# Kernel tuning notes

Hardware: AMD Instinct MI355X
Metric: run time of the kernel (lower is better)

The kernel has to match this reference:

```python
import jax, jax.numpy as jnp
import numpy as np

N = 100000
E = 1600000
D_IN = 128
HEADS = 4
C = 16  # hidden // heads
NEG_SLOPE = 0.2


def setup_inputs() -> dict:
    key = jax.random.key(0)
    ks = jax.random.split(key, 8)
    x = jax.random.normal(ks[0], (N, D_IN), dtype=jnp.float32)
    edge_index = jax.random.randint(ks[1], (2, E), 0, N, dtype=jnp.int32)
    s = 1.0 / np.sqrt(D_IN)
    W_l = jax.random.normal(ks[2], (D_IN, HEADS * C), dtype=jnp.float32) * s
    b_l = jnp.zeros((HEADS * C,), dtype=jnp.float32)
    W_r = jax.random.normal(ks[3], (D_IN, HEADS * C), dtype=jnp.float32) * s
    b_r = jnp.zeros((HEADS * C,), dtype=jnp.float32)
    att = jax.random.normal(ks[4], (HEADS, C), dtype=jnp.float32) * (1.0 / np.sqrt(C))
    bias = jnp.zeros((HEADS * C,), dtype=jnp.float32)
    W_head = jax.random.normal(ks[5], (HEADS * C, 1), dtype=jnp.float32) * (1.0 / np.sqrt(HEADS * C))
    b_head = jnp.zeros((1,), dtype=jnp.float32)
    return {"x": x, "edge_index": edge_index, "W_l": W_l, "b_l": b_l,
            "W_r": W_r, "b_r": b_r, "att": att, "bias": bias,
            "W_head": W_head, "b_head": b_head}


def reference(x, edge_index, W_l, b_l, W_r, b_r, att, bias, W_head, b_head):
    # GATv2Conv (PyG semantics, add_self_loops=True, concat=True)
    n = x.shape[0]
    # add self loops
    loops = jnp.arange(n, dtype=edge_index.dtype)
    src = jnp.concatenate([edge_index[0], loops])  # source j
    dst = jnp.concatenate([edge_index[1], loops])  # target i
    # per-node linear projections -> [N, H, C]
    x_l = (x @ W_l + b_l).reshape(n, HEADS, C)
    x_r = (x @ W_r + b_r).reshape(n, HEADS, C)
    # per-edge attention logits: att . LeakyReLU(x_l[j] + x_r[i])
    e = x_l[src] + x_r[dst]                               # [E', H, C]
    e = jnp.where(e >= 0, e, NEG_SLOPE * e)
    logits = jnp.einsum('ehc,hc->eh', e, att)             # [E', H]
    # segment softmax over incoming edges of each target node
    seg_max = jax.ops.segment_max(logits, dst, num_segments=n)  # [N, H]
    expw = jnp.exp(logits - seg_max[dst])
    seg_sum = jax.ops.segment_sum(expw, dst, num_segments=n)
    alpha = expw / seg_sum[dst]                           # [E', H]
    # weighted scatter-aggregate of source messages
    msg = alpha[:, :, None] * x_l[src]                    # [E', H, C]
    out = jax.ops.segment_sum(msg, dst, num_segments=n)   # [N, H, C]
    out = out.reshape(n, HEADS * C) + bias
    # ReLU + Linear head
    h = jax.nn.relu(out)
    return (h @ W_head + b_head).squeeze(-1)              # [N]
```

## Files before the change

### kernel.cpp

```cpp
#include <hip/hip_runtime.h>
#include <hip/hip_bf16.h>
#include <hip/hip_fp16.h>

#define HC 64
#define D_IN 128
#define NEG_SLOPE 0.2f
#define BCAP 8192

using f32x4 = __attribute__((ext_vector_type(4))) float;
using f16x8 = __attribute__((ext_vector_type(8))) _Float16;
using f16x2 = __attribute__((ext_vector_type(2))) _Float16;

__global__ void k_iota(int* __restrict__ p, int n) {
    int i = blockIdx.x * blockDim.x + threadIdx.x;
    if (i < n) p[i] = i * BCAP;
}

__global__ __launch_bounds__(256, 3) void k_proj(
    const float* __restrict__ x,
    const float* __restrict__ Wl, const float* __restrict__ bl,
    const float* __restrict__ Wr, const float* __restrict__ br,
    __half* __restrict__ xlh, float* __restrict__ xr, int N) {
    __shared__ _Float16 sWT[128 * 136];
    const int t = threadIdx.x;
    for (int idx = t; idx < 8192; idx += 256) {
        const int k = idx >> 6;
        const int c = idx & 63;
        sWT[c * 136 + k]        = (_Float16)Wl[idx];
        sWT[(c + 64) * 136 + k] = (_Float16)Wr[idx];
    }
    const int lane = t & 63;
    const int wave = t >> 6;
    const int m = lane & 15;
    const int q = lane >> 4;
    float bfu[8];
#pragma unroll
    for (int ct = 0; ct < 4; ++ct) bfu[ct] = bl[ct * 16 + m];
#pragma unroll
    for (int ct = 0; ct < 4; ++ct) bfu[4 + ct] = br[ct * 16 + m];
    __syncthreads();

    const int ntrip = N >> 5;
    for (int trip = blockIdx.x * 4 + wave; trip < ntrip; trip += gridDim.x * 4) {
        const int i0 = trip << 5;
        f16x8 af[2][4];
#pragma unroll
        for (int tt = 0; tt < 2; ++tt) {
            const float* xrow = x + (size_t)(i0 + tt * 16 + m) * D_IN + q * 8;
#pragma unroll
            for (int kk = 0; kk < 4; ++kk) {
                const float4* p4 = (const float4*)(xrow + kk * 32);
                float4 u = p4[0];
                float4 v = p4[1];
                f16x8 a;
                a[0] = (_Float16)u.x; a[1] = (_Float16)u.y;
                a[2] = (_Float16)u.z; a[3] = (_Float16)u.w;
                a[4] = (_Float16)v.x; a[5] = (_Float16)v.y;
                a[6] = (_Float16)v.z; a[7] = (_Float16)v.w;
                af[tt][kk] = a;
            }
        }
#pragma unroll
        for (int ct = 0; ct < 8; ++ct) {
            const _Float16* bp = &sWT[(ct * 16 + m) * 136 + q * 8];
            f32x4 acc0 = {0.f, 0.f, 0.f, 0.f};
            f32x4 acc1 = {0.f, 0.f, 0.f, 0.f};
#pragma unroll
            for (int kk = 0; kk < 4; ++kk) {
                f16x8 bf = *(const f16x8*)(bp + kk * 32);
                acc0 = __builtin_amdgcn_mfma_f32_16x16x32_f16(af[0][kk], bf, acc0, 0, 0, 0);
                acc1 = __builtin_amdgcn_mfma_f32_16x16x32_f16(af[1][kk], bf, acc1, 0, 0, 0);
            }
            const float bv = bfu[ct];
            if (ct < 4) {
                const int ch = ct * 16 + m;
#pragma unroll
                for (int r = 0; r < 4; ++r) {
                    xlh[(size_t)(i0 + q * 4 + r) * HC + ch]      = __float2half(acc0[r] + bv);
                    xlh[(size_t)(i0 + 16 + q * 4 + r) * HC + ch] = __float2half(acc1[r] + bv);
                }
            } else {
                const int ch = (ct - 4) * 16 + m;
#pragma unroll
                for (int r = 0; r < 4; ++r) {
                    xr[(size_t)(i0 + q * 4 + r) * HC + ch]      = acc0[r] + bv;
                    xr[(size_t)(i0 + 16 + q * 4 + r) * HC + ch] = acc1[r] + bv;
                }
            }
        }
    }
}


__global__ __launch_bounds__(256) void k_scat1(const int* __restrict__ src,
                                               const int* __restrict__ dst, int E,
                                               int* __restrict__ bfill,
                                               unsigned* __restrict__ coarse) {
    __shared__ int h[512], bl[512], cur[512];
    for (int t = threadIdx.x; t < 512; t += 256) { h[t] = 0; cur[t] = 0; }
    __syncthreads();
    const int beg = blockIdx.x * 8192;
    const int end = min(beg + 8192, E);
    for (int p = beg + threadIdx.x; p < end; p += 256)
        atomicAdd(&h[dst[p] >> 8], 1);
    __syncthreads();
    for (int t = threadIdx.x; t < 512; t += 256)
        bl[t] = h[t] ? atomicAdd(&bfill[t], h[t]) : 0;
    __syncthreads();
    for (int p = beg + threadIdx.x; p < end; p += 256) {
        const int d = dst[p];
        const int bin = d >> 8;
        const int r = atomicAdd(&cur[bin], 1);
        coarse[bl[bin] + r] = ((unsigned)src[p] << 8) | (unsigned)(d & 255);
    }
}

__global__ __launch_bounds__(256) void k_sort2(const unsigned* __restrict__ coarse,
                                               const int* __restrict__ bfill,
                                               int* __restrict__ row_off,
                                               int* __restrict__ endo,
                                               int* __restrict__ sorted_src, int N) {
    __shared__ int cnt[256], lds[256];
    const int t = threadIdx.x;
    const int b = blockIdx.x;
    const int eb = b * BCAP;
    const int ee = bfill[b];
    cnt[t] = 0;
    __syncthreads();
    for (int p = eb + t; p < ee; p += 256)
        atomicAdd(&cnt[coarse[p] & 255], 1);
    __syncthreads();
    const int c = cnt[t];
    lds[t] = c;
    __syncthreads();
    for (int o = 1; o < 256; o <<= 1) {
        int v = (t >= o) ? lds[t - o] : 0;
        __syncthreads();
        lds[t] += v;
        __syncthreads();
    }
    const int ex = lds[t] - c;
    const int node = (b << 8) + t;
    if (node < N) {
        row_off[node] = eb + ex;
        endo[node]    = eb + ex + c;
    }
    __syncthreads();
    cnt[t] = ex;
    __syncthreads();
    for (int p = eb + t; p < ee; p += 256) {
        const unsigned e = coarse[p];
        const int r = atomicAdd(&cnt[e & 255], 1);
        sorted_src[eb + r] = (int)(e >> 8);
    }
}

__device__ __forceinline__ float redhead8(float v) {
    int a;
    a = __builtin_amdgcn_update_dpp(0, __float_as_int(v), 0xB1, 0xF, 0xF, true);
    v += __int_as_float(a);
    a = __builtin_amdgcn_update_dpp(0, __float_as_int(v), 0x4E, 0xF, 0xF, true);
    v += __int_as_float(a);
    a = __builtin_amdgcn_update_dpp(0, __float_as_int(v), 0x141, 0xF, 0xF, true);
    v += __int_as_float(a);
    return v;
}

__global__ __launch_bounds__(256) void k_agg(
    const __half* __restrict__ xlh, const float* __restrict__ xr,
    const float* __restrict__ att, const float* __restrict__ bias,
    const float* __restrict__ Wh, const float* __restrict__ bh,
    const int* __restrict__ row_off, const int* __restrict__ endo,
    const int* __restrict__ sorted_src, float* __restrict__ out, int N) {
    const int wave = threadIdx.x >> 6;
    const int lane = threadIdx.x & 63;
    const int i = blockIdx.x * 4 + wave;
    if (i >= N) return;
    const int hl   = lane & 31;
    const int half = lane >> 5;

    const _Float16* xlhp = (const _Float16*)xlh;
    f16x2 att2;
    att2[0] = (_Float16)(att[2 * hl]     * 1.44269504f);
    att2[1] = (_Float16)(att[2 * hl + 1] * 1.44269504f);
    const f16x2 c02 = {(_Float16)NEG_SLOPE, (_Float16)NEG_SLOPE};

    const float2 xrf = *(const float2*)(xr + ((size_t)i << 6) + 2 * hl);
    f16x2 xri2; xri2[0] = (_Float16)xrf.x; xri2[1] = (_Float16)xrf.y;
    const f16x2 xli2 = *(const f16x2*)(xlhp + ((size_t)i << 6) + 2 * hl);

    f16x2 v0 = xli2 + xri2;
    v0 = __builtin_elementwise_max(v0, v0 * c02);
    float t0 = redhead8(__builtin_amdgcn_fdot2(att2, v0, 0.f, false));
    float p0 = exp2f(t0);
    float s = half ? 0.f : p0;
    float ax = half ? 0.f : p0 * (float)xli2[0];
    float ay = half ? 0.f : p0 * (float)xli2[1];

    int p = row_off[i];
    const int end = endo[i];

    for (; p + 8 <= end; p += 8) {
        int j[4]; f16x2 xv[4]; float tv[4];
#pragma unroll
        for (int r = 0; r < 4; ++r) j[r] = sorted_src[p + 2 * r + half];
#pragma unroll
        for (int r = 0; r < 4; ++r)
            xv[r] = *(const f16x2*)(xlhp + ((size_t)j[r] << 6) + 2 * hl);
#pragma unroll
        for (int r = 0; r < 4; ++r) {
            f16x2 v = xv[r] + xri2;
            v = __builtin_elementwise_max(v, v * c02);
            tv[r] = __builtin_amdgcn_fdot2(att2, v, 0.f, false);
        }
#pragma unroll
        for (int r = 0; r < 4; ++r) tv[r] = redhead8(tv[r]);
#pragma unroll
        for (int r = 0; r < 4; ++r) {
            float pe = exp2f(tv[r]);
            s += pe;
            ax = fmaf(pe, (float)xv[r][0], ax);
            ay = fmaf(pe, (float)xv[r][1], ay);
        }
    }
    for (; p + 2 <= end; p += 2) {
        int j = sorted_src[p + half];
        f16x2 xv = *(const f16x2*)(xlhp + ((size_t)j << 6) + 2 * hl);
        f16x2 v = xv + xri2;
        v = __builtin_elementwise_max(v, v * c02);
        float tt = redhead8(__builtin_amdgcn_fdot2(att2, v, 0.f, false));
        float pe = exp2f(tt);
        s += pe;
        ax = fmaf(pe, (float)xv[0], ax);
        ay = fmaf(pe, (float)xv[1], ay);
    }
    if (p < end) {
        int j = sorted_src[p];
        f16x2 xv = *(const f16x2*)(xlhp + ((size_t)j << 6) + 2 * hl);
        f16x2 v = xv + xri2;
        v = __builtin_elementwise_max(v, v * c02);
        float tt = redhead8(__builtin_amdgcn_fdot2(att2, v, 0.f, false));
        float pe = half ? 0.f : exp2f(tt);
        s += pe;
        ax = fmaf(pe, (float)xv[0], ax);
        ay = fmaf(pe, (float)xv[1], ay);
    }

    s  += __shfl_xor(s, 32);
    ax += __shfl_xor(ax, 32);
    ay += __shfl_xor(ay, 32);

    float ox = fmaxf(ax / s + bias[2 * hl],     0.f);
    float oy = fmaxf(ay / s + bias[2 * hl + 1], 0.f);
    float y = ox * Wh[2 * hl] + oy * Wh[2 * hl + 1];
    y += __shfl_xor(y, 1);
    y += __shfl_xor(y, 2);
    y += __shfl_xor(y, 4);
    y += __shfl_xor(y, 8);
    y += __shfl_xor(y, 16);
    y += __shfl_xor(y, 32);
    y *= 0.5f;
    if (lane == 0) out[i] = y + bh[0];
}

extern "C" void kernel_launch(void* const* d_in, const int* in_sizes, int n_in,
                              void* d_out, int out_size, void* d_ws, size_t ws_size,
                              hipStream_t stream) {
    const float* x   = (const float*)d_in[0];
    const int*   ei  = (const int*)d_in[1];
    const float* Wl  = (const float*)d_in[2];
    const float* bl  = (const float*)d_in[3];
    const float* Wr  = (const float*)d_in[4];
    const float* br  = (const float*)d_in[5];
    const float* att = (const float*)d_in[6];
    const float* bias= (const float*)d_in[7];
    const float* Wh  = (const float*)d_in[8];
    const float* bh  = (const float*)d_in[9];
    float* out = (float*)d_out;

    const int N = in_sizes[0] / D_IN;
    const int E = in_sizes[1] / 2;
    const int* src = ei;
    const int* dst = ei + E;
    const int nbkt = (N + 255) / 256;

    auto align = [](size_t v) { return (v + 255) & ~(size_t)255; };
    char* ws = (char*)d_ws;
    size_t off = 0;
    __half* xlh     = (__half*)(ws + off);   off = align(off + (size_t)N * HC * 2);
    float* xr       = (float*)(ws + off);    off = align(off + (size_t)N * HC * 4);
    int*   row_off  = (int*)(ws + off);      off = align(off + (size_t)N * 4);
    int*   endo     = (int*)(ws + off);      off = align(off + (size_t)N * 4);
    int*   bfill    = (int*)(ws + off);      off = align(off + 512 * 4);
    int*   sorted   = (int*)(ws + off);      off = align(off + (size_t)nbkt * BCAP * 4);
    unsigned* coarse= (unsigned*)(ws + off); off = align(off + (size_t)nbkt * BCAP * 4);
    (void)ws_size;

    k_iota<<<2, 256, 0, stream>>>(bfill, 512);

    k_proj<<<782, 256, 0, stream>>>(x, Wl, bl, Wr, br, xlh, xr, N);

    k_scat1<<<(E + 8191) / 8192, 256, 0, stream>>>(src, dst, E, bfill, coarse);
    k_sort2<<<nbkt, 256, 0, stream>>>(coarse, bfill, row_off, endo, sorted, N);

    k_agg<<<(N + 3) / 4, 256, 0, stream>>>(xlh, xr, att, bias, Wh, bh,
                                           row_off, endo, sorted, out, N);
}
```

Before: 234.6 us.

## Process four edges per wave with 16 lanes each and 8-byte loads

Remaps the aggregation wave from two 32-lane halves (2 channels per lane) to four 16-lane slots (4 channels per lane). Each lane now does 8-byte gathers, and the per-head reduction needs only two DPP steps, so four edges are in flight per wave step. Tail handling and the cross-slot reduction are rewritten to match. This trades fewer instructions per edge for more per-lane registers, and the 8-edge main loop loses its explicit batching of loads ahead of compute.

```diff
diff --git a/kernel.cpp b/kernel.cpp
--- a/kernel.cpp
+++ b/kernel.cpp
@@ -91,7 +91,6 @@
     }
 }
 
-
 __global__ __launch_bounds__(256) void k_scat1(const int* __restrict__ src,
                                                const int* __restrict__ dst, int E,
                                                int* __restrict__ bfill,
@@ -155,13 +154,11 @@
     }
 }
 
-__device__ __forceinline__ float redhead8(float v) {
+__device__ __forceinline__ float redquad(float v) {
     int a;
     a = __builtin_amdgcn_update_dpp(0, __float_as_int(v), 0xB1, 0xF, 0xF, true);
     v += __int_as_float(a);
     a = __builtin_amdgcn_update_dpp(0, __float_as_int(v), 0x4E, 0xF, 0xF, true);
-    v += __int_as_float(a);
-    a = __builtin_amdgcn_update_dpp(0, __float_as_int(v), 0x141, 0xF, 0xF, true);
     v += __int_as_float(a);
     return v;
 }
@@ -176,90 +173,95 @@
     const int lane = threadIdx.x & 63;
     const int i = blockIdx.x * 4 + wave;
     if (i >= N) return;
-    const int hl   = lane & 31;
-    const int half = lane >> 5;
+    const int sl   = lane & 15;
+    const int slot = lane >> 4;
 
     const _Float16* xlhp = (const _Float16*)xlh;
-    f16x2 att2;
-    att2[0] = (_Float16)(att[2 * hl]     * 1.44269504f);
-    att2[1] = (_Float16)(att[2 * hl + 1] * 1.44269504f);
+    const float4 attf = *(const float4*)(att + 4 * sl);
+    f16x2 attA, attB;
+    attA[0] = (_Float16)(attf.x * 1.44269504f);
+    attA[1] = (_Float16)(attf.y * 1.44269504f);
+    attB[0] = (_Float16)(attf.z * 1.44269504f);
+    attB[1] = (_Float16)(attf.w * 1.44269504f);
     const f16x2 c02 = {(_Float16)NEG_SLOPE, (_Float16)NEG_SLOPE};
 
-    const float2 xrf = *(const float2*)(xr + ((size_t)i << 6) + 2 * hl);
-    f16x2 xri2; xri2[0] = (_Float16)xrf.x; xri2[1] = (_Float16)xrf.y;
-    const f16x2 xli2 = *(const f16x2*)(xlhp + ((size_t)i << 6) + 2 * hl);
-
-    f16x2 v0 = xli2 + xri2;
-    v0 = __builtin_elementwise_max(v0, v0 * c02);
-    float t0 = redhead8(__builtin_amdgcn_fdot2(att2, v0, 0.f, false));
-    float p0 = exp2f(t0);
-    float s = half ? 0.f : p0;
-    float ax = half ? 0.f : p0 * (float)xli2[0];
-    float ay = half ? 0.f : p0 * (float)xli2[1];
+    const float4 xrf = *(const float4*)(xr + ((size_t)i << 6) + 4 * sl);
+    f16x2 xriA, xriB;
+    xriA[0] = (_Float16)xrf.x; xriA[1] = (_Float16)xrf.y;
+    xriB[0] = (_Float16)xrf.z; xriB[1] = (_Float16)xrf.w;
+    const uint2 xliraw = *(const uint2*)(xlhp + ((size_t)i << 6) + 4 * sl);
+    const f16x2 xliA = __builtin_bit_cast(f16x2, xliraw.x);
+    const f16x2 xliB = __builtin_bit_cast(f16x2, xliraw.y);
+
+    f16x2 vA = xliA + xriA, vB = xliB + xriB;
+    vA = __builtin_elementwise_max(vA, vA * c02);
+    vB = __builtin_elementwise_max(vB, vB * c02);
+    float t0 = redquad(__builtin_amdgcn_fdot2(attB, vB,
+                        __builtin_amdgcn_fdot2(attA, vA, 0.f, false), false));
+    float pe0 = (slot == 0) ? exp2f(t0) : 0.f;
+    float s  = pe0;
+    float a0 = pe0 * (float)xliA[0];
+    float a1 = pe0 * (float)xliA[1];
+    float a2 = pe0 * (float)xliB[0];
+    float a3 = pe0 * (float)xliB[1];
 
     int p = row_off[i];
     const int end = endo[i];
 
+#define EDGE_GROUP(JEXPR, PRED)                                              \
+    {                                                                        \
+        int jj = (JEXPR);                                                    \
+        uint2 raw = *(const uint2*)(xlhp + ((size_t)jj << 6) + 4 * sl);      \
+        f16x2 xA = __builtin_bit_cast(f16x2, raw.x);                         \
+        f16x2 xB = __builtin_bit_cast(f16x2, raw.y);                         \
+        f16x2 wA = xA + xriA, wB = xB + xriB;                                \
+        wA = __builtin_elementwise_max(wA, wA * c02);                        \
+        wB = __builtin_elementwise_max(wB, wB * c02);                        \
+        float tt = redquad(__builtin_amdgcn_fdot2(attB, wB,                  \
+                     __builtin_amdgcn_fdot2(attA, wA, 0.f, false), false));  \
+        float pe = (PRED) ? exp2f(tt) : 0.f;                                 \
+        s += pe;                                                             \
+        a0 = fmaf(pe, (float)xA[0], a0);                                     \
+        a1 = fmaf(pe, (float)xA[1], a1);                                     \
+        a2 = fmaf(pe, (float)xB[0], a2);                                     \
+        a3 = fmaf(pe, (float)xB[1], a3);                                     \
+    }
+
     for (; p + 8 <= end; p += 8) {
-        int j[4]; f16x2 xv[4]; float tv[4];
-#pragma unroll
-        for (int r = 0; r < 4; ++r) j[r] = sorted_src[p + 2 * r + half];
-#pragma unroll
-        for (int r = 0; r < 4; ++r)
-            xv[r] = *(const f16x2*)(xlhp + ((size_t)j[r] << 6) + 2 * hl);
-#pragma unroll
-        for (int r = 0; r < 4; ++r) {
-            f16x2 v = xv[r] + xri2;
-            v = __builtin_elementwise_max(v, v * c02);
-            tv[r] = __builtin_amdgcn_fdot2(att2, v, 0.f, false);
-        }
-#pragma unroll
-        for (int r = 0; r < 4; ++r) tv[r] = redhead8(tv[r]);
-#pragma unroll
-        for (int r = 0; r < 4; ++r) {
-            float pe = exp2f(tv[r]);
-            s += pe;
-            ax = fmaf(pe, (float)xv[r][0], ax);
-            ay = fmaf(pe, (float)xv[r][1], ay);
-        }
-    }
-    for (; p + 2 <= end; p += 2) {
-        int j = sorted_src[p + half];
-        f16x2 xv = *(const f16x2*)(xlhp + ((size_t)j << 6) + 2 * hl);
-        f16x2 v = xv + xri2;
-        v = __builtin_elementwise_max(v, v * c02);
-        float tt = redhead8(__builtin_amdgcn_fdot2(att2, v, 0.f, false));
-        float pe = exp2f(tt);
-        s += pe;
-        ax = fmaf(pe, (float)xv[0], ax);
-        ay = fmaf(pe, (float)xv[1], ay);
-    }
-    if (p < end) {
-        int j = sorted_src[p];
-        f16x2 xv = *(const f16x2*)(xlhp + ((size_t)j << 6) + 2 * hl);
-        f16x2 v = xv + xri2;
-        v = __builtin_elementwise_max(v, v * c02);
-        float tt = redhead8(__builtin_amdgcn_fdot2(att2, v, 0.f, false));
-        float pe = half ? 0.f : exp2f(tt);
-        s += pe;
-        ax = fmaf(pe, (float)xv[0], ax);
-        ay = fmaf(pe, (float)xv[1], ay);
-    }
-
-    s  += __shfl_xor(s, 32);
-    ax += __shfl_xor(ax, 32);
-    ay += __shfl_xor(ay, 32);
-
-    float ox = fmaxf(ax / s + bias[2 * hl],     0.f);
-    float oy = fmaxf(ay / s + bias[2 * hl + 1], 0.f);
-    float y = ox * Wh[2 * hl] + oy * Wh[2 * hl + 1];
+        int j0 = sorted_src[p + slot];
+        int j1 = sorted_src[p + 4 + slot];
+        EDGE_GROUP(j0, true)
+        EDGE_GROUP(j1, true)
+    }
+    if (p + 4 <= end) {
+        int j0 = sorted_src[p + slot];
+        EDGE_GROUP(j0, true)
+        p += 4;
+    }
+    const int rem = end - p;
+    if (rem > 0) {
+        int idx = p + slot;
+        int j0 = sorted_src[(idx < end) ? idx : (end - 1)];
+        EDGE_GROUP(j0, slot < rem)
+    }
+#undef EDGE_GROUP
+
+    s  += __shfl_xor(s, 16);  s  += __shfl_xor(s, 32);
+    a0 += __shfl_xor(a0, 16); a0 += __shfl_xor(a0, 32);
+    a1 += __shfl_xor(a1, 16); a1 += __shfl_xor(a1, 32);
+    a2 += __shfl_xor(a2, 16); a2 += __shfl_xor(a2, 32);
+    a3 += __shfl_xor(a3, 16); a3 += __shfl_xor(a3, 32);
+
+    const float4 bi = *(const float4*)(bias + 4 * sl);
+    const float4 wh = *(const float4*)(Wh + 4 * sl);
+    float y = fmaxf(a0 / s + bi.x, 0.f) * wh.x
+            + fmaxf(a1 / s + bi.y, 0.f) * wh.y
+            + fmaxf(a2 / s + bi.z, 0.f) * wh.z
+            + fmaxf(a3 / s + bi.w, 0.f) * wh.w;
     y += __shfl_xor(y, 1);
     y += __shfl_xor(y, 2);
     y += __shfl_xor(y, 4);
     y += __shfl_xor(y, 8);
-    y += __shfl_xor(y, 16);
-    y += __shfl_xor(y, 32);
-    y *= 0.5f;
     if (lane == 0) out[i] = y + bh[0];
 }
 
```

New measurement: 229.7 us. 1.02x faster.
